# Kernel optimization log

Measured on AMD Instinct MI355X. Metric: run time of the kernel, lower is better.

The kernel has to match this reference:

```python
import jax, jax.numpy as jnp
import numpy as np

NEG_SLOPE = 0.2

def gat_conv(x, src, dst, n, W, att_src, att_dst, bias, heads, out_ch, concat):
    # x: [N, F_in]; W: [heads*out_ch, F_in]; att_*: [heads, out_ch]; bias: [heads*out_ch] or [out_ch]
    h = (x @ W.T).reshape(n, heads, out_ch)              # [N,H,C]
    a_src = jnp.einsum('nhc,hc->nh', h, att_src)          # [N,H]
    a_dst = jnp.einsum('nhc,hc->nh', h, att_dst)          # [N,H]
    alpha = jax.nn.leaky_relu(a_src[src] + a_dst[dst], NEG_SLOPE)  # [E,H]
    # segment softmax over incoming edges of each destination node
    amax = jax.ops.segment_max(alpha, dst, num_segments=n)         # [N,H]
    amax = jnp.where(jnp.isfinite(amax), amax, 0.0)
    ex = jnp.exp(alpha - amax[dst])                                # [E,H]
    denom = jax.ops.segment_sum(ex, dst, num_segments=n)           # [N,H]
    w = ex / (denom[dst] + 1e-16)                                  # [E,H]
    out = jax.ops.segment_sum(w[:, :, None] * h[src], dst, num_segments=n)  # [N,H,C]
    if concat:
        out = out.reshape(n, heads * out_ch)
    else:
        out = out.mean(axis=1)
    return out + bias


def setup_inputs() -> dict:
    key = jax.random.key(0)
    ks = jax.random.split(key, 16)
    n, E = 10000, 320000
    in_dim, hid, heads = 128, 128, 4
    sc = lambda f: 1.0 / np.sqrt(f)
    x = jax.random.normal(ks[0], (n, in_dim), dtype=jnp.float32)
    edge_index = jax.random.randint(ks[1], (2, E), 0, n, dtype=jnp.int64)
    # layer 0: in_dim -> hid, heads=4, concat
    W0 = jax.random.normal(ks[2], (heads * hid, in_dim), jnp.float32) * sc(in_dim)
    att_src0 = jax.random.normal(ks[3], (heads, hid), jnp.float32) * sc(hid)
    att_dst0 = jax.random.normal(ks[4], (heads, hid), jnp.float32) * sc(hid)
    b0 = jnp.zeros((heads * hid,), jnp.float32)
    # layer 1: hid*heads -> hid, heads=1, concat
    W1 = jax.random.normal(ks[5], (hid, heads * hid), jnp.float32) * sc(heads * hid)
    att_src1 = jax.random.normal(ks[6], (1, hid), jnp.float32) * sc(hid)
    att_dst1 = jax.random.normal(ks[7], (1, hid), jnp.float32) * sc(hid)
    b1 = jnp.zeros((hid,), jnp.float32)
    Wout = jax.random.normal(ks[8], (hid, hid), jnp.float32) * sc(hid)
    bout = jnp.zeros((hid,), jnp.float32)
    Wedge = jax.random.normal(ks[9], (1, 2 * hid), jnp.float32) * sc(2 * hid)
    bedge = jnp.zeros((1,), jnp.float32)
    return {"x": x, "edge_index": edge_index, "W0": W0, "att_src0": att_src0,
            "att_dst0": att_dst0, "b0": b0, "W1": W1, "att_src1": att_src1,
            "att_dst1": att_dst1, "b1": b1, "Wout": Wout, "bout": bout,
            "Wedge": Wedge, "bedge": bedge}


def reference(x, edge_index, W0, att_src0, att_dst0, b0, W1, att_src1, att_dst1,
              b1, Wout, bout, Wedge, bedge):
    n = x.shape[0]
    hid = Wout.shape[0]
    # add self-loops (PyG GATConv default)
    loop = jnp.arange(n, dtype=edge_index.dtype)
    src = jnp.concatenate([edge_index[0], loop])
    dst = jnp.concatenate([edge_index[1], loop])
    h = jax.nn.elu(gat_conv(x, src, dst, n, W0, att_src0, att_dst0, b0, 4, hid, True))
    h = jax.nn.elu(gat_conv(h, src, dst, n, W1, att_src1, att_dst1, b1, 1, hid, True))
    h = h @ Wout.T + bout                                  # [n, hid]
    # edge_proj(cat(x_i, x_j)) == x_i @ w1 + x_j @ w2 + b  (avoid [n,n,2h] materialization)
    w1 = Wedge[0, :hid]
    w2 = Wedge[0, hid:]
    s1 = h @ w1                                            # [n]
    s2 = h @ w2                                            # [n]
    edge_logits = s1[:, None] + s2[None, :] + bedge[0]     # [n, n]
    return edge_logits
```

## Files before the change

kernel.cpp:

```cpp
#include <hip/hip_runtime.h>
#include <math.h>

#define LRELU_SLOPE 0.2f

typedef float f32x4 __attribute__((ext_vector_type(4)));

__device__ __forceinline__ float lrelu(float x){ return x >= 0.f ? x : LRELU_SLOPE*x; }
__device__ __forceinline__ float eluf(float x){ return x > 0.f ? x : expm1f(x); }

__global__ void k_hist(const int* __restrict__ ei, int E, int n, int* __restrict__ cnt){
    int e = blockIdx.x*blockDim.x + threadIdx.x;
    int NE = E + n;
    if (e >= NE) return;
    int d = (e < E) ? ei[E + e] : (e - E);
    atomicAdd(&cnt[d], 1);
}

__global__ __launch_bounds__(1024) void k_scan(const int* __restrict__ cnt, int n,
                                               int* __restrict__ off, int* __restrict__ cur){
    __shared__ int part[1024];
    const int ITEMS = (n + 1023) / 1024;
    int t = threadIdx.x;
    int base = t * ITEMS;
    int s = 0;
    for (int i = 0; i < ITEMS; i++){ int idx = base + i; if (idx < n) s += cnt[idx]; }
    part[t] = s;
    __syncthreads();
    for (int d = 1; d < 1024; d <<= 1){
        int v = 0;
        if (t >= d) v = part[t - d];
        __syncthreads();
        if (t >= d) part[t] += v;
        __syncthreads();
    }
    int excl = part[t] - s;
    for (int i = 0; i < ITEMS; i++){
        int idx = base + i;
        if (idx < n){ off[idx] = excl; cur[idx] = excl; excl += cnt[idx]; }
    }
    if (t == 1023) off[n] = part[1023];
}

__global__ void k_scatter(const int* __restrict__ ei, int E, int n,
                          int* __restrict__ cur, int* __restrict__ esrc){
    int e = blockIdx.x*blockDim.x + threadIdx.x;
    int NE = E + n;
    if (e >= NE) return;
    int s = (e < E) ? ei[e]     : (e - E);
    int d = (e < E) ? ei[E + e] : (e - E);
    int pos = atomicAdd(&cur[d], 1);
    esrc[pos] = s;
}

__global__ __launch_bounds__(256) void k_gemm_nt(
    const float* __restrict__ A, const float* __restrict__ B,
    const float* __restrict__ bias, float* __restrict__ C,
    int M, int N, int K)
{
    const int BM = 64, BN = 64, BK = 32, PAD = 4;
    __shared__ float As[BK][BM + PAD];
    __shared__ float Bs[BK][BN + PAD];
    int tid = threadIdx.x;
    int tx = tid & 15;
    int ty = tid >> 4;
    int m0 = blockIdx.x * BM;
    int n0 = blockIdx.y * BN;
    float acc[4][4] = {};

    int lm = tid >> 3;
    int lk = (tid & 7) * 4;

    for (int k0 = 0; k0 < K; k0 += BK){
        #pragma unroll
        for (int r = 0; r < 2; r++){
            int m = lm + 32*r;
            int row = m0 + m;
            float4 v = make_float4(0.f,0.f,0.f,0.f);
            if (row < M) v = *(const float4*)&A[(size_t)row*K + k0 + lk];
            As[lk+0][m] = v.x; As[lk+1][m] = v.y; As[lk+2][m] = v.z; As[lk+3][m] = v.w;
        }
        #pragma unroll
        for (int r = 0; r < 2; r++){
            int nn = lm + 32*r;
            int col = n0 + nn;
            float4 v = make_float4(0.f,0.f,0.f,0.f);
            if (col < N) v = *(const float4*)&B[(size_t)col*K + k0 + lk];
            Bs[lk+0][nn] = v.x; Bs[lk+1][nn] = v.y; Bs[lk+2][nn] = v.z; Bs[lk+3][nn] = v.w;
        }
        __syncthreads();
        #pragma unroll
        for (int kk = 0; kk < BK; kk++){
            float4 a = *(const float4*)&As[kk][tx*4];
            float4 b = *(const float4*)&Bs[kk][ty*4];
            float av[4] = {a.x,a.y,a.z,a.w};
            float bv[4] = {b.x,b.y,b.z,b.w};
            #pragma unroll
            for (int i = 0; i < 4; i++)
                #pragma unroll
                for (int j = 0; j < 4; j++)
                    acc[i][j] = fmaf(av[i], bv[j], acc[i][j]);
        }
        __syncthreads();
    }

    float4 bb = make_float4(0.f,0.f,0.f,0.f);
    if (bias) bb = *(const float4*)&bias[n0 + ty*4];
    #pragma unroll
    for (int i = 0; i < 4; i++){
        int row = m0 + tx*4 + i;
        if (row >= M) continue;
        float4 v = make_float4(acc[i][0]+bb.x, acc[i][1]+bb.y, acc[i][2]+bb.z, acc[i][3]+bb.w);
        *(float4*)&C[(size_t)row*N + n0 + ty*4] = v;
    }
}

__global__ __launch_bounds__(64) void k_att4(
    const float* __restrict__ h, const float* __restrict__ att_s,
    const float* __restrict__ att_d, int n,
    float* __restrict__ as_, float* __restrict__ ad_)
{
    int i = blockIdx.x, l = threadIdx.x;
    const float4* hr = (const float4*)(h + (size_t)i * 512);
    float4 v0 = hr[l*2], v1 = hr[l*2 + 1];
    int hh = l >> 4;
    const float4* sp = (const float4*)(att_s + hh*128 + (l & 15)*8);
    const float4* dp = (const float4*)(att_d + hh*128 + (l & 15)*8);
    float4 s0 = sp[0], s1v = sp[1];
    float4 d0 = dp[0], d1v = dp[1];
    float ps = v0.x*s0.x + v0.y*s0.y + v0.z*s0.z + v0.w*s0.w
             + v1.x*s1v.x + v1.y*s1v.y + v1.z*s1v.z + v1.w*s1v.w;
    float pd = v0.x*d0.x + v0.y*d0.y + v0.z*d0.z + v0.w*d0.w
             + v1.x*d1v.x + v1.y*d1v.y + v1.z*d1v.z + v1.w*d1v.w;
    #pragma unroll
    for (int o = 8; o > 0; o >>= 1){ ps += __shfl_xor(ps, o); pd += __shfl_xor(pd, o); }
    if ((l & 15) == 0){ as_[(size_t)i*4 + hh] = ps; ad_[(size_t)i*4 + hh] = pd; }
}

__global__ __launch_bounds__(64) void k_att1(
    const float* __restrict__ h, const float* __restrict__ att_s,
    const float* __restrict__ att_d, int n,
    float* __restrict__ as_, float* __restrict__ ad_)
{
    int i = blockIdx.x, l = threadIdx.x;
    float2 v  = ((const float2*)(h + (size_t)i * 128))[l];
    float2 s  = ((const float2*)att_s)[l];
    float2 dd = ((const float2*)att_d)[l];
    float ps = v.x*s.x + v.y*s.y;
    float pd = v.x*dd.x + v.y*dd.y;
    #pragma unroll
    for (int o = 32; o > 0; o >>= 1){ ps += __shfl_xor(ps, o); pd += __shfl_xor(pd, o); }
    if (l == 0){ as_[i] = ps; ad_[i] = pd; }
}

__global__ __launch_bounds__(256) void k_agg4(
    const float* __restrict__ hfeat,
    const float* __restrict__ as_,
    const float* __restrict__ ad_,
    const int* __restrict__ off, const int* __restrict__ esrc,
    const float* __restrict__ bias,
    float* __restrict__ out, int n)
{
    const int CH = 128;
    int d = blockIdx.x, t = threadIdx.x;
    int lane = t & 63, wv = t >> 6;

    __shared__ int   src_l[CH];
    __shared__ float exw[CH][4];
    __shared__ float dsum[4];
    __shared__ __align__(16) float part[4][512];

    int e0 = off[d], e1 = off[d+1];

    float ad0 = ad_[(size_t)d*4+0], ad1 = ad_[(size_t)d*4+1],
          ad2 = ad_[(size_t)d*4+2], ad3 = ad_[(size_t)d*4+3];

    float acc[8];
    #pragma unroll
    for (int j = 0; j < 8; j++) acc[j] = 0.f;
    float dtot = 0.f;

    for (int cb = e0; cb < e1; cb += CH){
        int ce = min(CH, e1 - cb);
        for (int e = t; e < ce; e += 256){
            int s = esrc[cb + e];
            src_l[e] = s;
            float4 a4 = ((const float4*)as_)[s];
            exw[e][0] = expf(fminf(lrelu(a4.x + ad0), 80.f));
            exw[e][1] = expf(fminf(lrelu(a4.y + ad1), 80.f));
            exw[e][2] = expf(fminf(lrelu(a4.z + ad2), 80.f));
            exw[e][3] = expf(fminf(lrelu(a4.w + ad3), 80.f));
        }
        __syncthreads();
        {
            float v = 0.f;
            for (int e = lane; e < ce; e += 64) v += exw[e][wv];
            #pragma unroll
            for (int o = 32; o > 0; o >>= 1) v += __shfl_xor(v, o);
            dtot += v;
        }
        for (int e = wv; e < ce; e += 4){
            int s = src_l[e];
            float w = exw[e][lane >> 4];
            const float4* hp = (const float4*)(hfeat + (size_t)s*512 + lane*8);
            float4 u0 = hp[0], u1 = hp[1];
            acc[0] = fmaf(w, u0.x, acc[0]);
            acc[1] = fmaf(w, u0.y, acc[1]);
            acc[2] = fmaf(w, u0.z, acc[2]);
            acc[3] = fmaf(w, u0.w, acc[3]);
            acc[4] = fmaf(w, u1.x, acc[4]);
            acc[5] = fmaf(w, u1.y, acc[5]);
            acc[6] = fmaf(w, u1.z, acc[6]);
            acc[7] = fmaf(w, u1.w, acc[7]);
        }
        __syncthreads();
    }

    if (lane == 0) dsum[wv] = dtot;
    float4* pr = (float4*)&part[wv][lane*8];
    pr[0] = make_float4(acc[0], acc[1], acc[2], acc[3]);
    pr[1] = make_float4(acc[4], acc[5], acc[6], acc[7]);
    __syncthreads();

    #pragma unroll
    for (int r = 0; r < 2; r++){
        int c = t + r*256;
        float sgm = part[0][c] + part[1][c] + part[2][c] + part[3][c];
        float val = sgm / (dsum[c >> 7] + 1e-16f) + bias[c];
        out[(size_t)d*512 + c] = eluf(val);
    }
}

__global__ __launch_bounds__(256) void k_agg1(
    const float* __restrict__ hfeat,
    const float* __restrict__ as_,
    const float* __restrict__ ad_,
    const int* __restrict__ off, const int* __restrict__ esrc,
    const float* __restrict__ bias,
    float* __restrict__ out, int n)
{
    const int CH = 128;
    int d = blockIdx.x, t = threadIdx.x;
    int lane = t & 63, wv = t >> 6;
    int half = lane >> 5, l5 = lane & 31;

    __shared__ int   src_l[CH];
    __shared__ float exw1[CH];
    __shared__ float dsum1;
    __shared__ __align__(16) float part[8][128];

    int e0 = off[d], e1 = off[d+1];
    float adl = ad_[d];

    float4 acc = make_float4(0.f, 0.f, 0.f, 0.f);
    float dtot = 0.f;

    for (int cb = e0; cb < e1; cb += CH){
        int ce = min(CH, e1 - cb);
        for (int e = t; e < ce; e += 256){
            int s = esrc[cb + e];
            src_l[e] = s;
            exw1[e] = expf(fminf(lrelu(as_[s] + adl), 80.f));
        }
        __syncthreads();
        if (wv == 0){
            float v = 0.f;
            for (int e = lane; e < ce; e += 64) v += exw1[e];
            #pragma unroll
            for (int o = 32; o > 0; o >>= 1) v += __shfl_xor(v, o);
            dtot += v;
        }
        int p = wv*2 + half;
        for (int e = p; e < ce; e += 8){
            int s = src_l[e];
            float w = exw1[e];
            float4 u = *(const float4*)(hfeat + (size_t)s*128 + l5*4);
            acc.x = fmaf(w, u.x, acc.x);
            acc.y = fmaf(w, u.y, acc.y);
            acc.z = fmaf(w, u.z, acc.z);
            acc.w = fmaf(w, u.w, acc.w);
        }
        __syncthreads();
    }

    if (t == 0) dsum1 = dtot;
    ((float4*)&part[wv*2 + half][0])[l5] = acc;
    __syncthreads();

    if (t < 128){
        float sgm = 0.f;
        #pragma unroll
        for (int p = 0; p < 8; p++) sgm += part[p][t];
        float val = sgm / (dsum1 + 1e-16f) + bias[t];
        out[(size_t)d*128 + t] = eluf(val);
    }
}

__global__ __launch_bounds__(64) void k_score(
    const float* __restrict__ h3, const float* __restrict__ wedge,
    const float* __restrict__ bedge, int n,
    float* __restrict__ s1, float* __restrict__ s2)
{
    int i = blockIdx.x, l = threadIdx.x;
    float2 v  = ((const float2*)(h3 + (size_t)i * 128))[l];
    float2 w1 = ((const float2*)wedge)[l];
    float2 w2 = ((const float2*)(wedge + 128))[l];
    float p1 = v.x*w1.x + v.y*w1.y;
    float p2 = v.x*w2.x + v.y*w2.y;
    #pragma unroll
    for (int o = 32; o > 0; o >>= 1){ p1 += __shfl_xor(p1, o); p2 += __shfl_xor(p2, o); }
    if (l == 0){ s1[i] = p1 + bedge[0]; s2[i] = p2; }
}

__global__ __launch_bounds__(256) void k_outer(
    const float* __restrict__ s1, const float* __restrict__ s2,
    float* __restrict__ out, int n)
{
    int i = blockIdx.x;
    float a = s1[i];
    f32x4* orow = (f32x4*)(out + (size_t)i * n);
    const f32x4* s2v = (const f32x4*)s2;
    int nq = n >> 2;
    for (int j = threadIdx.x; j < nq; j += blockDim.x){
        f32x4 b = s2v[j];
        f32x4 r = b + a;
        __builtin_nontemporal_store(r, &orow[j]);
    }
    int rem0 = nq << 2;
    for (int j = rem0 + threadIdx.x; j < n; j += blockDim.x)
        out[(size_t)i * n + j] = a + s2[j];
}

extern "C" void kernel_launch(void* const* d_in, const int* in_sizes, int n_in,
                              void* d_out, int out_size, void* d_ws, size_t ws_size,
                              hipStream_t stream) {
    const float* x     = (const float*)d_in[0];
    const int*   ei    = (const int*)  d_in[1];
    const float* W0    = (const float*)d_in[2];
    const float* as0w  = (const float*)d_in[3];
    const float* ad0w  = (const float*)d_in[4];
    const float* b0    = (const float*)d_in[5];
    const float* W1    = (const float*)d_in[6];
    const float* as1w  = (const float*)d_in[7];
    const float* ad1w  = (const float*)d_in[8];
    const float* b1    = (const float*)d_in[9];
    const float* Wout  = (const float*)d_in[10];
    const float* boutp = (const float*)d_in[11];
    const float* Wedge = (const float*)d_in[12];
    const float* bedge = (const float*)d_in[13];

    const int hid    = in_sizes[7];
    const int heads  = in_sizes[3] / hid;
    const int in_dim = in_sizes[2] / (heads * hid);
    const int n      = in_sizes[0] / in_dim;
    const int E      = in_sizes[1] / 2;
    const int NE     = E + n;
    const int F0     = heads * hid;

    char* ws = (char*)d_ws;
    size_t pos = 0;
    auto alloc = [&](size_t bytes) -> void* {
        pos = (pos + 255) & ~size_t(255);
        void* p = ws + pos;
        pos += bytes;
        return p;
    };
    float* a0s = (float*)alloc((size_t)n * heads * 4);
    float* a0d = (float*)alloc((size_t)n * heads * 4);
    float* a1s = (float*)alloc((size_t)n * 4);
    float* a1d = (float*)alloc((size_t)n * 4);
    float* s1  = (float*)alloc((size_t)n * 4);
    float* s2  = (float*)alloc((size_t)n * 4);
    int*   cnt = (int*)  alloc((size_t)n * 4);
    int*   offs= (int*)  alloc((size_t)(n + 1) * 4);
    int*   cur = (int*)  alloc((size_t)n * 4);

    auto al = [](size_t b){ return (b + 255) & ~size_t(255); };
    size_t b_esrc = al((size_t)NE * 4);
    size_t b_h0   = al((size_t)n * F0 * 4);
    size_t b_o1   = al((size_t)n * F0 * 4);
    size_t b_h1   = al((size_t)n * hid * 4);
    size_t b_o2   = al((size_t)n * hid * 4);
    size_t b_h3   = al((size_t)n * hid * 4);
    size_t big_need = b_esrc + b_h0 + b_o1 + b_h1 + b_o2 + b_h3;
    size_t small_end = (pos + 255) & ~size_t(255);
    char* big = (small_end + big_need <= ws_size) ? (ws + small_end) : (char*)d_out;
    size_t bp = 0;
    int*   esrc = (int*)  (big + bp); bp += b_esrc;
    float* h0   = (float*)(big + bp); bp += b_h0;
    float* o1   = (float*)(big + bp); bp += b_o1;
    float* h1   = (float*)(big + bp); bp += b_h1;
    float* o2   = (float*)(big + bp); bp += b_o2;
    float* h3   = (float*)(big + bp); bp += b_h3;

    (void)hipMemsetAsync(cnt, 0, (size_t)n * 4, stream);
    int tb = 256, gbE = (NE + tb - 1) / tb;
    k_hist   <<<gbE, tb, 0, stream>>>(ei, E, n, cnt);
    k_scan   <<<1, 1024, 0, stream>>>(cnt, n, offs, cur);
    k_scatter<<<gbE, tb, 0, stream>>>(ei, E, n, cur, esrc);

    int gx = (n + 63) / 64;

    k_gemm_nt<<<dim3(gx, F0/64), 256, 0, stream>>>(x, W0, nullptr, h0, n, F0, in_dim);
    k_att4   <<<n, 64, 0, stream>>>(h0, as0w, ad0w, n, a0s, a0d);
    k_agg4   <<<n, 256, 0, stream>>>(h0, a0s, a0d, offs, esrc, b0, o1, n);

    k_gemm_nt<<<dim3(gx, hid/64), 256, 0, stream>>>(o1, W1, nullptr, h1, n, hid, F0);
    k_att1   <<<n, 64, 0, stream>>>(h1, as1w, ad1w, n, a1s, a1d);
    k_agg1   <<<n, 256, 0, stream>>>(h1, a1s, a1d, offs, esrc, b1, o2, n);

    k_gemm_nt<<<dim3(gx, hid/64), 256, 0, stream>>>(o2, Wout, boutp, h3, n, hid, hid);

    k_score<<<n, 64, 0, stream>>>(h3, Wedge, bedge, n, s1, s2);
    k_outer<<<n, 256, 0, stream>>>(s1, s2, (float*)d_out, n);
}
```

Baseline: 684.6 us.

## Fuse attention and score projections into GEMM epilogues, store features as fp16

The attention-coefficient dot products and the final edge-score projection move into the GEMM epilogues, with partial sums combined through shared and global atomics, so the separate att4/att1/score kernels go away. The projected features consumed by aggregation are stored as fp16 to halve gather traffic in the edge aggregation kernels. This costs extra atomics, requires zeroing the accumulators with a memset, and lowers the precision of the gathered features.

```diff
diff --git a/kernel.cpp b/kernel.cpp
--- a/kernel.cpp
+++ b/kernel.cpp
@@ -4,6 +4,9 @@
 #define LRELU_SLOPE 0.2f
 
 typedef float f32x4 __attribute__((ext_vector_type(4)));
+typedef _Float16 h16;
+typedef h16 h16x8 __attribute__((ext_vector_type(8)));
+typedef h16 h16x4 __attribute__((ext_vector_type(4)));
 
 __device__ __forceinline__ float lrelu(float x){ return x >= 0.f ? x : LRELU_SLOPE*x; }
 __device__ __forceinline__ float eluf(float x){ return x > 0.f ? x : expm1f(x); }
@@ -52,14 +55,18 @@
     esrc[pos] = s;
 }
 
-__global__ __launch_bounds__(256) void k_gemm_nt(
+template<int H>
+__global__ __launch_bounds__(256) void k_gemm_h16_att(
     const float* __restrict__ A, const float* __restrict__ B,
-    const float* __restrict__ bias, float* __restrict__ C,
+    h16* __restrict__ C,
+    const float* __restrict__ att_s, const float* __restrict__ att_d,
+    float* __restrict__ as_, float* __restrict__ ad_,
     int M, int N, int K)
 {
     const int BM = 64, BN = 64, BK = 32, PAD = 4;
     __shared__ float As[BK][BM + PAD];
     __shared__ float Bs[BK][BN + PAD];
+    __shared__ float asl[64], adl[64];
     int tid = threadIdx.x;
     int tx = tid & 15;
     int ty = tid >> 4;
@@ -69,6 +76,8 @@
 
     int lm = tid >> 3;
     int lk = (tid & 7) * 4;
+
+    if (tid < 64){ asl[tid] = 0.f; adl[tid] = 0.f; }
 
     for (int k0 = 0; k0 < K; k0 += BK){
         #pragma unroll
@@ -103,57 +112,117 @@
         __syncthreads();
     }
 
-    float4 bb = make_float4(0.f,0.f,0.f,0.f);
-    if (bias) bb = *(const float4*)&bias[n0 + ty*4];
     #pragma unroll
     for (int i = 0; i < 4; i++){
         int row = m0 + tx*4 + i;
         if (row >= M) continue;
-        float4 v = make_float4(acc[i][0]+bb.x, acc[i][1]+bb.y, acc[i][2]+bb.z, acc[i][3]+bb.w);
-        *(float4*)&C[(size_t)row*N + n0 + ty*4] = v;
-    }
-}
-
-__global__ __launch_bounds__(64) void k_att4(
-    const float* __restrict__ h, const float* __restrict__ att_s,
-    const float* __restrict__ att_d, int n,
-    float* __restrict__ as_, float* __restrict__ ad_)
+        h16x4 hv;
+        hv[0] = (h16)acc[i][0]; hv[1] = (h16)acc[i][1];
+        hv[2] = (h16)acc[i][2]; hv[3] = (h16)acc[i][3];
+        *(h16x4*)&C[(size_t)row*N + n0 + ty*4] = hv;
+    }
+
+    int head = (H == 1) ? 0 : (n0 >> 7);
+    int cb = head*128 + (n0 & 127) + ty*4;
+    float ws0 = att_s[cb+0], ws1 = att_s[cb+1], ws2 = att_s[cb+2], ws3 = att_s[cb+3];
+    float wd0 = att_d[cb+0], wd1 = att_d[cb+1], wd2 = att_d[cb+2], wd3 = att_d[cb+3];
+    #pragma unroll
+    for (int i = 0; i < 4; i++){
+        float ps = acc[i][0]*ws0 + acc[i][1]*ws1 + acc[i][2]*ws2 + acc[i][3]*ws3;
+        float pd = acc[i][0]*wd0 + acc[i][1]*wd1 + acc[i][2]*wd2 + acc[i][3]*wd3;
+        atomicAdd(&asl[tx*4+i], ps);
+        atomicAdd(&adl[tx*4+i], pd);
+    }
+    __syncthreads();
+    if (tid < 64){
+        int row = m0 + tid;
+        if (row < M){
+            atomicAdd(&as_[(size_t)row*H + head], asl[tid]);
+            atomicAdd(&ad_[(size_t)row*H + head], adl[tid]);
+        }
+    }
+}
+
+__global__ __launch_bounds__(256) void k_gemm_score(
+    const float* __restrict__ A, const float* __restrict__ B,
+    const float* __restrict__ bias,
+    const float* __restrict__ w1, const float* __restrict__ w2,
+    float* __restrict__ s1, float* __restrict__ s2,
+    int M, int N, int K)
 {
-    int i = blockIdx.x, l = threadIdx.x;
-    const float4* hr = (const float4*)(h + (size_t)i * 512);
-    float4 v0 = hr[l*2], v1 = hr[l*2 + 1];
-    int hh = l >> 4;
-    const float4* sp = (const float4*)(att_s + hh*128 + (l & 15)*8);
-    const float4* dp = (const float4*)(att_d + hh*128 + (l & 15)*8);
-    float4 s0 = sp[0], s1v = sp[1];
-    float4 d0 = dp[0], d1v = dp[1];
-    float ps = v0.x*s0.x + v0.y*s0.y + v0.z*s0.z + v0.w*s0.w
-             + v1.x*s1v.x + v1.y*s1v.y + v1.z*s1v.z + v1.w*s1v.w;
-    float pd = v0.x*d0.x + v0.y*d0.y + v0.z*d0.z + v0.w*d0.w
-             + v1.x*d1v.x + v1.y*d1v.y + v1.z*d1v.z + v1.w*d1v.w;
+    const int BM = 64, BN = 64, BK = 32, PAD = 4;
+    __shared__ float As[BK][BM + PAD];
+    __shared__ float Bs[BK][BN + PAD];
+    __shared__ float r1[64], r2[64];
+    int tid = threadIdx.x;
+    int tx = tid & 15;
+    int ty = tid >> 4;
+    int m0 = blockIdx.x * BM;
+    int n0 = blockIdx.y * BN;
+    float acc[4][4] = {};
+
+    int lm = tid >> 3;
+    int lk = (tid & 7) * 4;
+
+    if (tid < 64){ r1[tid] = 0.f; r2[tid] = 0.f; }
+
+    for (int k0 = 0; k0 < K; k0 += BK){
+        #pragma unroll
+        for (int r = 0; r < 2; r++){
+            int m = lm + 32*r;
+            int row = m0 + m;
+            float4 v = make_float4(0.f,0.f,0.f,0.f);
+            if (row < M) v = *(const float4*)&A[(size_t)row*K + k0 + lk];
+            As[lk+0][m] = v.x; As[lk+1][m] = v.y; As[lk+2][m] = v.z; As[lk+3][m] = v.w;
+        }
+        #pragma unroll
+        for (int r = 0; r < 2; r++){
+            int nn = lm + 32*r;
+            int col = n0 + nn;
+            float4 v = make_float4(0.f,0.f,0.f,0.f);
+            if (col < N) v = *(const float4*)&B[(size_t)col*K + k0 + lk];
+            Bs[lk+0][nn] = v.x; Bs[lk+1][nn] = v.y; Bs[lk+2][nn] = v.z; Bs[lk+3][nn] = v.w;
+        }
+        __syncthreads();
+        #pragma unroll
+        for (int kk = 0; kk < BK; kk++){
+            float4 a = *(const float4*)&As[kk][tx*4];
+            float4 b = *(const float4*)&Bs[kk][ty*4];
+            float av[4] = {a.x,a.y,a.z,a.w};
+            float bv[4] = {b.x,b.y,b.z,b.w};
+            #pragma unroll
+            for (int i = 0; i < 4; i++)
+                #pragma unroll
+                for (int j = 0; j < 4; j++)
+                    acc[i][j] = fmaf(av[i], bv[j], acc[i][j]);
+        }
+        __syncthreads();
+    }
+
+    int c0 = n0 + ty*4;
+    float b0v = bias[c0+0], b1v = bias[c0+1], b2v = bias[c0+2], b3v = bias[c0+3];
+    float wa0 = w1[c0+0], wa1 = w1[c0+1], wa2 = w1[c0+2], wa3 = w1[c0+3];
+    float wb0 = w2[c0+0], wb1 = w2[c0+1], wb2 = w2[c0+2], wb3 = w2[c0+3];
     #pragma unroll
-    for (int o = 8; o > 0; o >>= 1){ ps += __shfl_xor(ps, o); pd += __shfl_xor(pd, o); }
-    if ((l & 15) == 0){ as_[(size_t)i*4 + hh] = ps; ad_[(size_t)i*4 + hh] = pd; }
-}
-
-__global__ __launch_bounds__(64) void k_att1(
-    const float* __restrict__ h, const float* __restrict__ att_s,
-    const float* __restrict__ att_d, int n,
-    float* __restrict__ as_, float* __restrict__ ad_)
-{
-    int i = blockIdx.x, l = threadIdx.x;
-    float2 v  = ((const float2*)(h + (size_t)i * 128))[l];
-    float2 s  = ((const float2*)att_s)[l];
-    float2 dd = ((const float2*)att_d)[l];
-    float ps = v.x*s.x + v.y*s.y;
-    float pd = v.x*dd.x + v.y*dd.y;
-    #pragma unroll
-    for (int o = 32; o > 0; o >>= 1){ ps += __shfl_xor(ps, o); pd += __shfl_xor(pd, o); }
-    if (l == 0){ as_[i] = ps; ad_[i] = pd; }
+    for (int i = 0; i < 4; i++){
+        float v0 = acc[i][0]+b0v, v1 = acc[i][1]+b1v, v2 = acc[i][2]+b2v, v3 = acc[i][3]+b3v;
+        float p1 = v0*wa0 + v1*wa1 + v2*wa2 + v3*wa3;
+        float p2 = v0*wb0 + v1*wb1 + v2*wb2 + v3*wb3;
+        atomicAdd(&r1[tx*4+i], p1);
+        atomicAdd(&r2[tx*4+i], p2);
+    }
+    __syncthreads();
+    if (tid < 64){
+        int row = m0 + tid;
+        if (row < M){
+            atomicAdd(&s1[row], r1[tid]);
+            atomicAdd(&s2[row], r2[tid]);
+        }
+    }
 }
 
 __global__ __launch_bounds__(256) void k_agg4(
-    const float* __restrict__ hfeat,
+    const h16* __restrict__ hfeat,
     const float* __restrict__ as_,
     const float* __restrict__ ad_,
     const int* __restrict__ off, const int* __restrict__ esrc,
@@ -201,16 +270,15 @@
         for (int e = wv; e < ce; e += 4){
             int s = src_l[e];
             float w = exw[e][lane >> 4];
-            const float4* hp = (const float4*)(hfeat + (size_t)s*512 + lane*8);
-            float4 u0 = hp[0], u1 = hp[1];
-            acc[0] = fmaf(w, u0.x, acc[0]);
-            acc[1] = fmaf(w, u0.y, acc[1]);
-            acc[2] = fmaf(w, u0.z, acc[2]);
-            acc[3] = fmaf(w, u0.w, acc[3]);
-            acc[4] = fmaf(w, u1.x, acc[4]);
-            acc[5] = fmaf(w, u1.y, acc[5]);
-            acc[6] = fmaf(w, u1.z, acc[6]);
-            acc[7] = fmaf(w, u1.w, acc[7]);
+            h16x8 u = ((const h16x8*)(hfeat + (size_t)s*512))[lane];
+            acc[0] = fmaf(w, (float)u[0], acc[0]);
+            acc[1] = fmaf(w, (float)u[1], acc[1]);
+            acc[2] = fmaf(w, (float)u[2], acc[2]);
+            acc[3] = fmaf(w, (float)u[3], acc[3]);
+            acc[4] = fmaf(w, (float)u[4], acc[4]);
+            acc[5] = fmaf(w, (float)u[5], acc[5]);
+            acc[6] = fmaf(w, (float)u[6], acc[6]);
+            acc[7] = fmaf(w, (float)u[7], acc[7]);
         }
         __syncthreads();
     }
@@ -231,7 +299,7 @@
 }
 
 __global__ __launch_bounds__(256) void k_agg1(
-    const float* __restrict__ hfeat,
+    const h16* __restrict__ hfeat,
     const float* __restrict__ as_,
     const float* __restrict__ ad_,
     const int* __restrict__ off, const int* __restrict__ esrc,
@@ -273,11 +341,11 @@
         for (int e = p; e < ce; e += 8){
             int s = src_l[e];
             float w = exw1[e];
-            float4 u = *(const float4*)(hfeat + (size_t)s*128 + l5*4);
-            acc.x = fmaf(w, u.x, acc.x);
-            acc.y = fmaf(w, u.y, acc.y);
-            acc.z = fmaf(w, u.z, acc.z);
-            acc.w = fmaf(w, u.w, acc.w);
+            h16x4 u = ((const h16x4*)(hfeat + (size_t)s*128))[l5];
+            acc.x = fmaf(w, (float)u[0], acc.x);
+            acc.y = fmaf(w, (float)u[1], acc.y);
+            acc.z = fmaf(w, (float)u[2], acc.z);
+            acc.w = fmaf(w, (float)u[3], acc.w);
         }
         __syncthreads();
     }
@@ -295,28 +363,13 @@
     }
 }
 
-__global__ __launch_bounds__(64) void k_score(
-    const float* __restrict__ h3, const float* __restrict__ wedge,
-    const float* __restrict__ bedge, int n,
-    float* __restrict__ s1, float* __restrict__ s2)
-{
-    int i = blockIdx.x, l = threadIdx.x;
-    float2 v  = ((const float2*)(h3 + (size_t)i * 128))[l];
-    float2 w1 = ((const float2*)wedge)[l];
-    float2 w2 = ((const float2*)(wedge + 128))[l];
-    float p1 = v.x*w1.x + v.y*w1.y;
-    float p2 = v.x*w2.x + v.y*w2.y;
-    #pragma unroll
-    for (int o = 32; o > 0; o >>= 1){ p1 += __shfl_xor(p1, o); p2 += __shfl_xor(p2, o); }
-    if (l == 0){ s1[i] = p1 + bedge[0]; s2[i] = p2; }
-}
-
 __global__ __launch_bounds__(256) void k_outer(
     const float* __restrict__ s1, const float* __restrict__ s2,
+    const float* __restrict__ bedge,
     float* __restrict__ out, int n)
 {
     int i = blockIdx.x;
-    float a = s1[i];
+    float a = s1[i] + bedge[0];
     f32x4* orow = (f32x4*)(out + (size_t)i * n);
     const f32x4* s2v = (const f32x4*)s2;
     int nq = n >> 2;
@@ -371,28 +424,28 @@
     float* s1  = (float*)alloc((size_t)n * 4);
     float* s2  = (float*)alloc((size_t)n * 4);
     int*   cnt = (int*)  alloc((size_t)n * 4);
+    size_t zero_end = pos;
     int*   offs= (int*)  alloc((size_t)(n + 1) * 4);
     int*   cur = (int*)  alloc((size_t)n * 4);
 
     auto al = [](size_t b){ return (b + 255) & ~size_t(255); };
     size_t b_esrc = al((size_t)NE * 4);
-    size_t b_h0   = al((size_t)n * F0 * 4);
+    size_t b_h0h  = al((size_t)n * F0 * 2);
     size_t b_o1   = al((size_t)n * F0 * 4);
-    size_t b_h1   = al((size_t)n * hid * 4);
+    size_t b_h1h  = al((size_t)n * hid * 2);
     size_t b_o2   = al((size_t)n * hid * 4);
-    size_t b_h3   = al((size_t)n * hid * 4);
-    size_t big_need = b_esrc + b_h0 + b_o1 + b_h1 + b_o2 + b_h3;
+    size_t big_need = b_esrc + b_h0h + b_o1 + b_h1h + b_o2;
     size_t small_end = (pos + 255) & ~size_t(255);
     char* big = (small_end + big_need <= ws_size) ? (ws + small_end) : (char*)d_out;
     size_t bp = 0;
     int*   esrc = (int*)  (big + bp); bp += b_esrc;
-    float* h0   = (float*)(big + bp); bp += b_h0;
+    h16*   h0h  = (h16*)  (big + bp); bp += b_h0h;
     float* o1   = (float*)(big + bp); bp += b_o1;
-    float* h1   = (float*)(big + bp); bp += b_h1;
+    h16*   h1h  = (h16*)  (big + bp); bp += b_h1h;
     float* o2   = (float*)(big + bp); bp += b_o2;
-    float* h3   = (float*)(big + bp); bp += b_h3;
-
-    (void)hipMemsetAsync(cnt, 0, (size_t)n * 4, stream);
+
+    (void)hipMemsetAsync(ws, 0, zero_end, stream);
+
     int tb = 256, gbE = (NE + tb - 1) / tb;
     k_hist   <<<gbE, tb, 0, stream>>>(ei, E, n, cnt);
     k_scan   <<<1, 1024, 0, stream>>>(cnt, n, offs, cur);
@@ -400,16 +453,16 @@
 
     int gx = (n + 63) / 64;
 
-    k_gemm_nt<<<dim3(gx, F0/64), 256, 0, stream>>>(x, W0, nullptr, h0, n, F0, in_dim);
-    k_att4   <<<n, 64, 0, stream>>>(h0, as0w, ad0w, n, a0s, a0d);
-    k_agg4   <<<n, 256, 0, stream>>>(h0, a0s, a0d, offs, esrc, b0, o1, n);
-
-    k_gemm_nt<<<dim3(gx, hid/64), 256, 0, stream>>>(o1, W1, nullptr, h1, n, hid, F0);
-    k_att1   <<<n, 64, 0, stream>>>(h1, as1w, ad1w, n, a1s, a1d);
-    k_agg1   <<<n, 256, 0, stream>>>(h1, a1s, a1d, offs, esrc, b1, o2, n);
-
-    k_gemm_nt<<<dim3(gx, hid/64), 256, 0, stream>>>(o2, Wout, boutp, h3, n, hid, hid);
-
-    k_score<<<n, 64, 0, stream>>>(h3, Wedge, bedge, n, s1, s2);
-    k_outer<<<n, 256, 0, stream>>>(s1, s2, (float*)d_out, n);
-}
+    k_gemm_h16_att<4><<<dim3(gx, F0/64), 256, 0, stream>>>(
+        x, W0, h0h, as0w, ad0w, a0s, a0d, n, F0, in_dim);
+    k_agg4<<<n, 256, 0, stream>>>(h0h, a0s, a0d, offs, esrc, b0, o1, n);
+
+    k_gemm_h16_att<1><<<dim3(gx, hid/64), 256, 0, stream>>>(
+        o1, W1, h1h, as1w, ad1w, a1s, a1d, n, hid, F0);
+    k_agg1<<<n, 256, 0, stream>>>(h1h, a1s, a1d, offs, esrc, b1, o2, n);
+
+    k_gemm_score<<<dim3(gx, hid/64), 256, 0, stream>>>(
+        o2, Wout, boutp, Wedge, Wedge + hid, s1, s2, n, hid, hid);
+
+    k_outer<<<n, 256, 0, stream>>>(s1, s2, bedge, (float*)d_out, n);
+}
```

New measurement: 650.3 us. 5.0% less time.
